# Kernel tuning notes

Measured on AMD Instinct MI355X. Metric: run time of the kernel, lower is better.

The kernel has to match this reference:

```python
import jax, jax.numpy as jnp
import numpy as np
import math

D_MODEL = 512
NUM_HEADS = 8
D_HEAD = D_MODEL // NUM_HEADS
B, S = 8, 1024


def _rel_shift(pos_score):
    # pos_score: [B, H, S, S] -> Transformer-XL relative shift
    b, h, s1, s2 = pos_score.shape
    padded = jnp.concatenate([jnp.zeros((b, h, s1, 1), pos_score.dtype), pos_score], axis=-1)
    padded = padded.reshape(b, h, s2 + 1, s1)
    return padded[:, :, 1:].reshape(b, h, s1, s2)


def setup_inputs() -> dict:
    key = jax.random.key(0)
    ks = jax.random.split(key, 16)
    scale = 1.0 / math.sqrt(D_MODEL)
    inp = {
        'query': jax.random.normal(ks[0], (B, S, D_MODEL), jnp.float32),
        'key': jax.random.normal(ks[1], (B, S, D_MODEL), jnp.float32),
        'value': jax.random.normal(ks[2], (B, S, D_MODEL), jnp.float32),
        'position_emb': jax.random.normal(ks[3], (B, S, D_MODEL), jnp.float32),
        'Wq': jax.random.normal(ks[4], (D_MODEL, D_MODEL), jnp.float32) * scale,
        'bq': jnp.zeros((D_MODEL,), jnp.float32),
        'Wk': jax.random.normal(ks[5], (D_MODEL, D_MODEL), jnp.float32) * scale,
        'bk': jnp.zeros((D_MODEL,), jnp.float32),
        'Wv': jax.random.normal(ks[6], (D_MODEL, D_MODEL), jnp.float32) * scale,
        'bv': jnp.zeros((D_MODEL,), jnp.float32),
        'Wp': jax.random.normal(ks[7], (D_MODEL, D_MODEL), jnp.float32) * scale,
        'u_bias': jax.random.normal(ks[8], (NUM_HEADS, D_HEAD), jnp.float32) * 0.1,
        'v_bias': jax.random.normal(ks[9], (NUM_HEADS, D_HEAD), jnp.float32) * 0.1,
        'Wo': jax.random.normal(ks[10], (D_MODEL, D_MODEL), jnp.float32) * scale,
        'bo': jnp.zeros((D_MODEL,), jnp.float32),
    }
    return inp


def reference(query, key, value, position_emb, Wq, bq, Wk, bk, Wv, bv, Wp, u_bias, v_bias, Wo, bo):
    b, s, _ = query.shape
    q = (query @ Wq + bq).reshape(b, s, NUM_HEADS, D_HEAD)       # [B,S,H,Dh]
    k = (key @ Wk + bk).reshape(b, s, NUM_HEADS, D_HEAD)
    v = (value @ Wv + bv).reshape(b, s, NUM_HEADS, D_HEAD)
    p = (position_emb @ Wp).reshape(b, s, NUM_HEADS, D_HEAD)
    # content score: (q + u) k^T ; pos score: (q + v) p^T with relative shift
    content_score = jnp.einsum('bqhd,bkhd->bhqk', q + u_bias, k)
    pos_score = _rel_shift(jnp.einsum('bqhd,bkhd->bhqk', q + v_bias, p))
    score = (content_score + pos_score) / math.sqrt(D_MODEL)
    atten = jax.nn.softmax(score, axis=-1)                        # dropout off (eval)
    context = jnp.einsum('bhqk,bkhd->bqhd', atten, v).reshape(b, s, D_MODEL)
    return context @ Wo + bo
```

## Files before the change

kernel.cpp:

```cpp
#include <hip/hip_runtime.h>
#include <cstdint>

typedef unsigned short ushort_t;
typedef __attribute__((ext_vector_type(8))) short bf16x8;
typedef __attribute__((ext_vector_type(4))) float f32x4;

#define S_LEN 1024
#define DHEAD 64

__device__ inline ushort_t f2bf(float f) {
    union { float f; uint32_t u; } c; c.f = f;
    uint32_t u = c.u;
    uint32_t r = u + 0x7FFFu + ((u >> 16) & 1u);
    return (ushort_t)(r >> 16);
}
__device__ inline float bf2f(ushort_t h) {
    union { uint32_t u; float f; } c; c.u = ((uint32_t)h) << 16;
    return c.f;
}
__device__ inline bf16x8 load8(const ushort_t* p) {
    union { uint4 u; bf16x8 v; } c;
    c.u = *reinterpret_cast<const uint4*>(p);
    return c.v;
}

__global__ __launch_bounds__(256) void prep_w(
    const float* __restrict__ wq, const float* __restrict__ wk,
    const float* __restrict__ wv, const float* __restrict__ wp,
    const float* __restrict__ wo, ushort_t* __restrict__ ws) {
    __shared__ float tile[64][65];
    int wi = blockIdx.z;
    const float* src = wi == 0 ? wq : wi == 1 ? wk : wi == 2 ? wv : wi == 3 ? wp : wo;
    int cx = blockIdx.x * 64, ry = blockIdx.y * 64;
    int t = threadIdx.x;
    int tr = t >> 4, tc = (t & 15) * 4;
#pragma unroll
    for (int i = 0; i < 4; i++) {
        int r = tr + i * 16;
        float4 f = *reinterpret_cast<const float4*>(src + (size_t)(ry + r) * 512 + cx + tc);
        tile[r][tc] = f.x; tile[r][tc + 1] = f.y; tile[r][tc + 2] = f.z; tile[r][tc + 3] = f.w;
    }
    __syncthreads();
    ushort_t* dst = ws + (size_t)wi * 262144;
#pragma unroll
    for (int i = 0; i < 4; i++) {
        int r = tr + i * 16;
        ushort4 o;
        o.x = f2bf(tile[tc][r]); o.y = f2bf(tile[tc + 1][r]);
        o.z = f2bf(tile[tc + 2][r]); o.w = f2bf(tile[tc + 3][r]);
        *reinterpret_cast<ushort4*>(dst + (size_t)(cx + r) * 512 + ry + tc) = o;
    }
}

__global__ __launch_bounds__(256) void prep_act(
    const float* __restrict__ q, const float* __restrict__ k,
    const float* __restrict__ v, const float* __restrict__ p,
    ushort_t* __restrict__ actb) {
    int t = blockIdx.x * 256 + threadIdx.x;
    int sec = blockIdx.y;
    const float* src = sec == 0 ? q : sec == 1 ? k : sec == 2 ? v : p;
    ushort_t* dst = actb + (size_t)sec * 4194304;
    float4 f = reinterpret_cast<const float4*>(src)[t];
    ushort4 o;
    o.x = f2bf(f.x); o.y = f2bf(f.y); o.z = f2bf(f.z); o.w = f2bf(f.w);
    *reinterpret_cast<ushort4*>(dst + (size_t)t * 4) = o;
}

template<int CVT>
__global__ __launch_bounds__(256) void proj_gemm(
    const float* __restrict__ qa, const float* __restrict__ ka,
    const float* __restrict__ va, const float* __restrict__ pa,
    const ushort_t* __restrict__ actb,
    const ushort_t* __restrict__ wT,
    const float* __restrict__ bq, const float* __restrict__ bk,
    const float* __restrict__ bv,
    const float* __restrict__ ub, const float* __restrict__ vb,
    ushort_t* __restrict__ Qu, ushort_t* __restrict__ Qv,
    ushort_t* __restrict__ Kp, ushort_t* __restrict__ Pp,
    ushort_t* __restrict__ Vt) {
    __shared__ ushort_t smem[2][128][72];
    int z = blockIdx.z;
    const float* Af = z == 0 ? qa : z == 1 ? ka : z == 2 ? pa : va;
    const ushort_t* Ab = actb + (size_t)(z == 0 ? 0 : z == 1 ? 1 : z == 2 ? 3 : 2) * 4194304;
    const ushort_t* Bt = wT + (z == 0 ? 0 : z == 1 ? 262144 : z == 2 ? 786432 : 524288);
    const float* bias = z == 0 ? bq : z == 1 ? bk : z == 3 ? bv : nullptr;

    int tid = threadIdx.x;
    int wid = tid >> 6, lane = tid & 63, quad = lane >> 4, l16 = lane & 15;
    int wr = wid >> 1, wc = wid & 1;
    int row0 = blockIdx.y * 128, col0 = blockIdx.x * 128;

    f32x4 acc[4][4];
#pragma unroll
    for (int i = 0; i < 4; i++)
#pragma unroll
        for (int j = 0; j < 4; j++) acc[i][j] = (f32x4){0.f, 0.f, 0.f, 0.f};

    for (int k0 = 0; k0 < 512; k0 += 64) {
#pragma unroll
        for (int i = 0; i < 4; i++) {
            int cid = tid + i * 256;
            int r = cid >> 3, c8 = cid & 7;
            if (CVT) {
                const float* ap = Af + (size_t)(row0 + r) * 512 + k0 + c8 * 8;
                float4 f0 = *reinterpret_cast<const float4*>(ap);
                float4 f1 = *reinterpret_cast<const float4*>(ap + 4);
                union { ushort_t s[8]; uint4 u; } pk;
                pk.s[0] = f2bf(f0.x); pk.s[1] = f2bf(f0.y); pk.s[2] = f2bf(f0.z); pk.s[3] = f2bf(f0.w);
                pk.s[4] = f2bf(f1.x); pk.s[5] = f2bf(f1.y); pk.s[6] = f2bf(f1.z); pk.s[7] = f2bf(f1.w);
                *reinterpret_cast<uint4*>(&smem[0][r][c8 * 8]) = pk.u;
            } else {
                *reinterpret_cast<uint4*>(&smem[0][r][c8 * 8]) =
                    *reinterpret_cast<const uint4*>(Ab + (size_t)(row0 + r) * 512 + k0 + c8 * 8);
            }
            *reinterpret_cast<uint4*>(&smem[1][r][c8 * 8]) =
                *reinterpret_cast<const uint4*>(Bt + (size_t)(col0 + r) * 512 + k0 + c8 * 8);
        }
        __syncthreads();
#pragma unroll
        for (int kc = 0; kc < 2; kc++) {
            bf16x8 af[4], bg[4];
#pragma unroll
            for (int m = 0; m < 4; m++)
                af[m] = load8(&smem[0][wr * 64 + m * 16 + l16][kc * 32 + quad * 8]);
#pragma unroll
            for (int n = 0; n < 4; n++)
                bg[n] = load8(&smem[1][wc * 64 + n * 16 + l16][kc * 32 + quad * 8]);
#pragma unroll
            for (int m = 0; m < 4; m++)
#pragma unroll
                for (int n = 0; n < 4; n++)
                    acc[m][n] = __builtin_amdgcn_mfma_f32_16x16x32_bf16(af[m], bg[n], acc[m][n], 0, 0, 0);
        }
        __syncthreads();
    }

    if (z == 3) {
        ushort_t (*Ts)[130] = reinterpret_cast<ushort_t(*)[130]>(&smem[0][0][0]);
#pragma unroll
        for (int m = 0; m < 4; m++)
#pragma unroll
            for (int n = 0; n < 4; n++) {
                int dl = wc * 64 + n * 16 + l16;
                float bcol = bv[col0 + dl];
#pragma unroll
                for (int r = 0; r < 4; r++) {
                    int sl = wr * 64 + m * 16 + quad * 4 + r;
                    Ts[dl][sl] = f2bf(acc[m][n][r] + bcol);
                }
            }
        __syncthreads();
        int b_ = row0 >> 10, s0 = row0 & 1023;
#pragma unroll
        for (int p = 0; p < 8; p++) {
            int dl = p * 16 + (tid >> 4);
            int sl = (tid & 15) * 8;
            int col = col0 + dl, h_ = col >> 6, d_ = col & 63;
            ushort_t* dst = Vt + (((size_t)(b_ * 8 + h_)) * 64 + d_) * 1024 + s0 + sl;
            union { uint4 u; ushort_t s[8]; } pk;
#pragma unroll
            for (int e = 0; e < 8; e++) pk.s[e] = Ts[dl][sl + e];
            *reinterpret_cast<uint4*>(dst) = pk.u;
        }
    } else {
#pragma unroll
        for (int m = 0; m < 4; m++)
#pragma unroll
            for (int n = 0; n < 4; n++) {
                int col = col0 + wc * 64 + n * 16 + l16;
                float bcol = bias ? bias[col] : 0.f;
#pragma unroll
                for (int r = 0; r < 4; r++) {
                    int row = row0 + wr * 64 + m * 16 + quad * 4 + r;
                    float val = acc[m][n][r] + bcol;
                    int b_ = row >> 10, s_ = row & 1023, h_ = col >> 6, d_ = col & 63;
                    size_t idx = (((size_t)(b_ * 8 + h_)) * 1024 + s_) * 64 + d_;
                    if (z == 0) {
                        Qu[idx] = f2bf(val + ub[col]);
                        Qv[idx] = f2bf(val + vb[col]);
                    } else {
                        (z == 1 ? Kp : Pp)[idx] = f2bf(val);
                    }
                }
            }
    }
}

__global__ __launch_bounds__(256) void out_gemm(
    const ushort_t* __restrict__ A, const ushort_t* __restrict__ Bt,
    const float* __restrict__ bias, float* __restrict__ outf) {
    __shared__ ushort_t As[128][72];
    __shared__ ushort_t Bs[64][72];
    int tid = threadIdx.x;
    int wid = tid >> 6, lane = tid & 63, quad = lane >> 4, l16 = lane & 15;
    int row0 = blockIdx.y * 128, col0 = blockIdx.x * 64;

    f32x4 acc[2][4];
#pragma unroll
    for (int i = 0; i < 2; i++)
#pragma unroll
        for (int j = 0; j < 4; j++) acc[i][j] = (f32x4){0.f, 0.f, 0.f, 0.f};

    for (int k0 = 0; k0 < 512; k0 += 64) {
#pragma unroll
        for (int i = 0; i < 4; i++) {
            int cid = tid + i * 256;
            int r = cid >> 3, c8 = cid & 7;
            *reinterpret_cast<uint4*>(&As[r][c8 * 8]) =
                *reinterpret_cast<const uint4*>(A + (size_t)(row0 + r) * 512 + k0 + c8 * 8);
        }
#pragma unroll
        for (int i = 0; i < 2; i++) {
            int cid = tid + i * 256;
            int r = cid >> 3, c8 = cid & 7;
            *reinterpret_cast<uint4*>(&Bs[r][c8 * 8]) =
                *reinterpret_cast<const uint4*>(Bt + (size_t)(col0 + r) * 512 + k0 + c8 * 8);
        }
        __syncthreads();
#pragma unroll
        for (int kc = 0; kc < 2; kc++) {
            bf16x8 af[2], bg[4];
#pragma unroll
            for (int m = 0; m < 2; m++)
                af[m] = load8(&As[wid * 32 + m * 16 + l16][kc * 32 + quad * 8]);
#pragma unroll
            for (int n = 0; n < 4; n++)
                bg[n] = load8(&Bs[n * 16 + l16][kc * 32 + quad * 8]);
#pragma unroll
            for (int m = 0; m < 2; m++)
#pragma unroll
                for (int n = 0; n < 4; n++)
                    acc[m][n] = __builtin_amdgcn_mfma_f32_16x16x32_bf16(af[m], bg[n], acc[m][n], 0, 0, 0);
        }
        __syncthreads();
    }
#pragma unroll
    for (int m = 0; m < 2; m++)
#pragma unroll
        for (int n = 0; n < 4; n++) {
            int col = col0 + n * 16 + l16;
#pragma unroll
            for (int r = 0; r < 4; r++) {
                int row = row0 + wid * 32 + m * 16 + quad * 4 + r;
                outf[(size_t)row * 512 + col] = acc[m][n][r] + bias[col];
            }
        }
}

#define POS_EMIT(B0_, B1_, WT_) do {                                          \
    f32x4 acc_ = (f32x4){0.f, 0.f, 0.f, 0.f};                                 \
    acc_ = __builtin_amdgcn_mfma_f32_16x16x32_bf16(av[0], (B0_), acc_, 0, 0, 0); \
    acc_ = __builtin_amdgcn_mfma_f32_16x16x32_bf16(av[1], (B1_), acc_, 0, 0, 0); \
    int kb_ = (WT_) + kbb;                                                    \
    if (kb_ >= kw0 && kb_ + 30 < kw1 && (WT_) + 15 <= collim) {               \
        _Pragma("unroll") for (int r_ = 0; r_ < 4; r_++) {                    \
            int m_ = quad * 4 + r_;                                           \
            sc[mtrow + m_][kb_ + m_ + l16] = f2bf(acc_[r_]);                  \
        }                                                                     \
    } else {                                                                  \
        _Pragma("unroll") for (int r_ = 0; r_ < 4; r_++) {                    \
            int m_ = quad * 4 + r_;                                           \
            int k_ = kb_ + m_ + l16;                                          \
            if (k_ >= kw0 && k_ < kw1 && ((WT_) + l16) <= collim)             \
                sc[mtrow + m_][k_] = f2bf(acc_[r_]);                          \
        }                                                                     \
    }                                                                         \
} while (0)

__device__ __forceinline__ void pos_pass(
    const ushort_t* __restrict__ P_b, ushort_t (*sc)[1032],
    const bf16x8* av, int wlo, int whi, int kbb, int collim, int mtrow,
    int kw0, int kw1, int quad, int l16) {
    if (whi < wlo) return;
    int nw = (whi - wlo) / 16 + 1;
    bf16x8 A0, A1, B0, B1;
    {
        int pr = wlo + l16; if (pr > S_LEN - 1) pr = S_LEN - 1;
        A0 = load8(P_b + (size_t)pr * 64 + quad * 8);
        A1 = load8(P_b + (size_t)pr * 64 + 32 + quad * 8);
    }
    if (nw > 1) {
        int pr = wlo + 16 + l16; if (pr > S_LEN - 1) pr = S_LEN - 1;
        B0 = load8(P_b + (size_t)pr * 64 + quad * 8);
        B1 = load8(P_b + (size_t)pr * 64 + 32 + quad * 8);
    }
    int w = 0;
    for (; w + 1 < nw; w += 2) {
        int wtA = wlo + w * 16;
        POS_EMIT(A0, A1, wtA);
        if (w + 2 < nw) {
            int pr = wtA + 32 + l16; if (pr > S_LEN - 1) pr = S_LEN - 1;
            A0 = load8(P_b + (size_t)pr * 64 + quad * 8);
            A1 = load8(P_b + (size_t)pr * 64 + 32 + quad * 8);
        }
        int wtB = wtA + 16;
        POS_EMIT(B0, B1, wtB);
        if (w + 3 < nw) {
            int pr = wtB + 32 + l16; if (pr > S_LEN - 1) pr = S_LEN - 1;
            B0 = load8(P_b + (size_t)pr * 64 + quad * 8);
            B1 = load8(P_b + (size_t)pr * 64 + 32 + quad * 8);
        }
    }
    if (w < nw) {
        int wt = wlo + w * 16;
        POS_EMIT(A0, A1, wt);
    }
}

__global__ __launch_bounds__(256, 2) void attn_kernel(
    const ushort_t* __restrict__ Qu, const ushort_t* __restrict__ Qv,
    const ushort_t* __restrict__ Kp, const ushort_t* __restrict__ Pp,
    const ushort_t* __restrict__ Vt, ushort_t* __restrict__ ctxb) {
    __shared__ ushort_t sc[32][1032];
    __shared__ float red1[4][32];
    __shared__ float red2[32][8];
    __shared__ float rowinv[32];

    constexpr float SCL = (float)(1.4426950408889634 / 22.627416997969522);

    int i = blockIdx.x;
    int bh = (i & 7) * 8 + (i >> 8);
    int q0 = ((i >> 3) & 31) << 5;

    int tid = threadIdx.x, wid = tid >> 6, lane = tid & 63;
    int quad = lane >> 4, l16 = lane & 15;

    const ushort_t* Qu_b = Qu + (size_t)bh * S_LEN * DHEAD;
    const ushort_t* Qv_b = Qv + (size_t)bh * S_LEN * DHEAD;
    const ushort_t* K_b  = Kp + (size_t)bh * S_LEN * DHEAD;
    const ushort_t* P_b  = Pp + (size_t)bh * S_LEN * DHEAD;
    const ushort_t* V_b  = Vt + (size_t)bh * DHEAD * S_LEN;

    int kw0 = wid << 8, kw1 = kw0 + 256;
    int d0 = wid << 4;

    bf16x8 au0[2], au1[2];
#pragma unroll
    for (int kc = 0; kc < 2; kc++) {
        au0[kc] = load8(Qu_b + (size_t)(q0 + l16) * 64 + kc * 32 + quad * 8);
        au1[kc] = load8(Qu_b + (size_t)(q0 + 16 + l16) * 64 + kc * 32 + quad * 8);
    }

    if (lane < 32) {
        int kz = q0 + lane + 1;
        if (kz >= kw0 && kz < kw1) sc[lane][kz] = 0;
    }

#pragma unroll
    for (int mt = 0; mt < 2; mt++) {
        int q0m = q0 + mt * 16;
        bf16x8 av1[2], av2[2];
#pragma unroll
        for (int kc = 0; kc < 2; kc++) {
            av1[kc] = load8(Qv_b + (size_t)(q0m + l16) * 64 + kc * 32 + quad * 8);
            int r2 = q0m + 1 + l16; if (r2 > S_LEN - 1) r2 = S_LEN - 1;
            av2[kc] = load8(Qv_b + (size_t)r2 * 64 + kc * 32 + quad * 8);
        }
        int wlo = (S_LEN - 16) - q0m + kw0;
        int d1 = kw1 - 1 - q0m; if (d1 > 0) d1 = 0;
        int whi = (S_LEN - 1) + d1;
        pos_pass(P_b, sc, av1, wlo, whi, q0m - (S_LEN - 1), S_LEN - 1,
                 mt * 16, kw0, kw1, quad, l16);
        int wlo2 = kw0 - q0m - 17; if (wlo2 < 0) wlo2 = 0;
        int whi2 = kw1 - 3 - q0m;
        pos_pass(P_b, sc, av2, wlo2, whi2, q0m + 2, 1 << 30,
                 mt * 16, kw0, kw1, quad, l16);
    }

    float pm0[4] = {-1e30f, -1e30f, -1e30f, -1e30f};
    float pm1[4] = {-1e30f, -1e30f, -1e30f, -1e30f};
    const ushort_t* Kw = K_b + (size_t)kw0 * 64;
#pragma unroll
    for (int nt = 0; nt < 16; ++nt) {
        const ushort_t* kp = Kw + (size_t)(nt * 16 + l16) * 64;
        bf16x8 b0 = load8(kp + quad * 8);
        bf16x8 b1 = load8(kp + 32 + quad * 8);
        int kt = kw0 + nt * 16;
        f32x4 a0, a1;
#pragma unroll
        for (int r = 0; r < 4; r++) {
            a0[r] = bf2f(sc[quad * 4 + r][kt + l16]);
            a1[r] = bf2f(sc[16 + quad * 4 + r][kt + l16]);
        }
        a0 = __builtin_amdgcn_mfma_f32_16x16x32_bf16(au0[0], b0, a0, 0, 0, 0);
        a0 = __builtin_amdgcn_mfma_f32_16x16x32_bf16(au0[1], b1, a0, 0, 0, 0);
        a1 = __builtin_amdgcn_mfma_f32_16x16x32_bf16(au1[0], b0, a1, 0, 0, 0);
        a1 = __builtin_amdgcn_mfma_f32_16x16x32_bf16(au1[1], b1, a1, 0, 0, 0);
#pragma unroll
        for (int r = 0; r < 4; r++) {
            sc[quad * 4 + r][kt + l16] = f2bf(a0[r]);
            sc[16 + quad * 4 + r][kt + l16] = f2bf(a1[r]);
            pm0[r] = fmaxf(pm0[r], a0[r]);
            pm1[r] = fmaxf(pm1[r], a1[r]);
        }
    }
#pragma unroll
    for (int off = 1; off < 16; off <<= 1)
#pragma unroll
        for (int r = 0; r < 4; r++) {
            pm0[r] = fmaxf(pm0[r], __shfl_xor(pm0[r], off));
            pm1[r] = fmaxf(pm1[r], __shfl_xor(pm1[r], off));
        }
    if (l16 == 0) {
#pragma unroll
        for (int r = 0; r < 4; r++) {
            red1[wid][quad * 4 + r] = pm0[r];
            red1[wid][16 + quad * 4 + r] = pm1[r];
        }
    }
    __syncthreads();

    int row = tid & 31, cb = tid >> 5;
    float rm = fmaxf(fmaxf(red1[0][row], red1[1][row]), fmaxf(red1[2][row], red1[3][row]));
    float ssum = 0.f;
    ushort_t* sp = &sc[row][cb * 128];
#pragma unroll
    for (int j = 0; j < 16; j++) {
        union { uint4 u; ushort_t s[8]; } in, out;
        in.u = *reinterpret_cast<uint4*>(sp + j * 8);
#pragma unroll
        for (int e = 0; e < 8; e++) {
            float ev = exp2f((bf2f(in.s[e]) - rm) * SCL);
            out.s[e] = f2bf(ev);
            ssum += ev;
        }
        *reinterpret_cast<uint4*>(sp + j * 8) = out.u;
    }
    red2[row][cb] = ssum;
    __syncthreads();
    if (tid < 32) {
        float s = 0.f;
#pragma unroll
        for (int c = 0; c < 8; c++) s += red2[tid][c];
        rowinv[tid] = 1.0f / s;
    }

    const ushort_t* Vw = V_b + (size_t)(d0 + l16) * 1024;
    f32x4 ac0 = (f32x4){0.f, 0.f, 0.f, 0.f};
    f32x4 ac1 = (f32x4){0.f, 0.f, 0.f, 0.f};
#pragma unroll
    for (int kc = 0; kc < 32; ++kc) {
        bf16x8 b = load8(Vw + kc * 32 + quad * 8);
        bf16x8 a0 = load8(&sc[l16][kc * 32 + quad * 8]);
        bf16x8 a1 = load8(&sc[16 + l16][kc * 32 + quad * 8]);
        ac0 = __builtin_amdgcn_mfma_f32_16x16x32_bf16(a0, b, ac0, 0, 0, 0);
        ac1 = __builtin_amdgcn_mfma_f32_16x16x32_bf16(a1, b, ac1, 0, 0, 0);
    }
    __syncthreads();
    int b_ = bh >> 3, h_ = bh & 7;
#pragma unroll
    for (int r = 0; r < 4; r++) {
        int m = quad * 4 + r;
        ctxb[((size_t)b_ * 1024 + (q0 + m)) * 512 + h_ * 64 + d0 + l16] =
            f2bf(ac0[r] * rowinv[m]);
        ctxb[((size_t)b_ * 1024 + (q0 + 16 + m)) * 512 + h_ * 64 + d0 + l16] =
            f2bf(ac1[r] * rowinv[16 + m]);
    }
}

extern "C" void kernel_launch(void* const* d_in, const int* in_sizes, int n_in,
                              void* d_out, int out_size, void* d_ws, size_t ws_size,
                              hipStream_t stream) {
    const float* q  = (const float*)d_in[0];
    const float* k  = (const float*)d_in[1];
    const float* v  = (const float*)d_in[2];
    const float* pe = (const float*)d_in[3];
    const float* Wq = (const float*)d_in[4];
    const float* bq = (const float*)d_in[5];
    const float* Wk = (const float*)d_in[6];
    const float* bk = (const float*)d_in[7];
    const float* Wv = (const float*)d_in[8];
    const float* bv = (const float*)d_in[9];
    const float* Wp = (const float*)d_in[10];
    const float* ub = (const float*)d_in[11];
    const float* vbias = (const float*)d_in[12];
    const float* Wo = (const float*)d_in[13];
    const float* bo = (const float*)d_in[14];
    float* out = (float*)d_out;
    ushort_t* ws = (ushort_t*)d_ws;

    ushort_t* wT  = ws;
    ushort_t* Qu  = ws + 1310720;
    ushort_t* Qv  = Qu + 4194304;
    ushort_t* Kp  = Qv + 4194304;
    ushort_t* Pp  = Kp + 4194304;
    ushort_t* Vt  = Pp + 4194304;
    ushort_t* actb = Vt + 4194304;
    ushort_t* ctx_big = actb;

    const size_t need_big = (size_t)(1310720 + 9 * 4194304) * 2;
    bool big = ws_size >= need_big;

    prep_w<<<dim3(8, 8, 5), 256, 0, stream>>>(Wq, Wk, Wv, Wp, Wo, wT);
    if (big) {
        prep_act<<<dim3(4096, 4), 256, 0, stream>>>(q, k, v, pe, actb);
        proj_gemm<0><<<dim3(4, 64, 4), 256, 0, stream>>>(q, k, v, pe, actb, wT,
            bq, bk, bv, ub, vbias, Qu, Qv, Kp, Pp, Vt);
        attn_kernel<<<2048, 256, 0, stream>>>(Qu, Qv, Kp, Pp, Vt, ctx_big);
        out_gemm<<<dim3(8, 64), 256, 0, stream>>>(ctx_big, wT + 4 * 262144, bo, out);
    } else {
        ushort_t* ctx = actb;
        proj_gemm<1><<<dim3(4, 64, 4), 256, 0, stream>>>(q, k, v, pe, nullptr, wT,
            bq, bk, bv, ub, vbias, Qu, Qv, Kp, Pp, Vt);
        attn_kernel<<<2048, 256, 0, stream>>>(Qu, Qv, Kp, Pp, Vt, ctx);
        out_gemm<<<dim3(8, 64), 256, 0, stream>>>(ctx, wT + 4 * 262144, bo, out);
    }
}
```

Before: 328.1 us.

## Fuse fp32 conversion into projection, async LDS loads in out_gemm, register softmax

Drops the separate activation-conversion kernel and always converts fp32 inputs to bf16 inside the projection GEMM's tile load, removing one launch and a round trip of bf16 activations through memory. The output GEMM now fills shared memory with direct global-to-LDS async loads, which requires unpadded tiles and may add bank conflicts. The attention kernel keeps score tiles in registers, computes exp and row sums there, and writes only the probabilities to shared memory. This avoids a second read-modify-write pass over the score buffer at the cost of higher register pressure.

```diff
diff --git a/kernel.cpp b/kernel.cpp
--- a/kernel.cpp
+++ b/kernel.cpp
@@ -22,6 +22,11 @@
     union { uint4 u; bf16x8 v; } c;
     c.u = *reinterpret_cast<const uint4*>(p);
     return c.v;
+}
+__device__ __forceinline__ void async16(const ushort_t* g, ushort_t* l) {
+    __builtin_amdgcn_global_load_lds(
+        (const __attribute__((address_space(1))) uint32_t*)(const void*)g,
+        (__attribute__((address_space(3))) uint32_t*)(void*)l, 16, 0, 0);
 }
 
 __global__ __launch_bounds__(256) void prep_w(
@@ -52,25 +57,9 @@
     }
 }
 
-__global__ __launch_bounds__(256) void prep_act(
-    const float* __restrict__ q, const float* __restrict__ k,
-    const float* __restrict__ v, const float* __restrict__ p,
-    ushort_t* __restrict__ actb) {
-    int t = blockIdx.x * 256 + threadIdx.x;
-    int sec = blockIdx.y;
-    const float* src = sec == 0 ? q : sec == 1 ? k : sec == 2 ? v : p;
-    ushort_t* dst = actb + (size_t)sec * 4194304;
-    float4 f = reinterpret_cast<const float4*>(src)[t];
-    ushort4 o;
-    o.x = f2bf(f.x); o.y = f2bf(f.y); o.z = f2bf(f.z); o.w = f2bf(f.w);
-    *reinterpret_cast<ushort4*>(dst + (size_t)t * 4) = o;
-}
-
-template<int CVT>
 __global__ __launch_bounds__(256) void proj_gemm(
     const float* __restrict__ qa, const float* __restrict__ ka,
     const float* __restrict__ va, const float* __restrict__ pa,
-    const ushort_t* __restrict__ actb,
     const ushort_t* __restrict__ wT,
     const float* __restrict__ bq, const float* __restrict__ bk,
     const float* __restrict__ bv,
@@ -81,7 +70,6 @@
     __shared__ ushort_t smem[2][128][72];
     int z = blockIdx.z;
     const float* Af = z == 0 ? qa : z == 1 ? ka : z == 2 ? pa : va;
-    const ushort_t* Ab = actb + (size_t)(z == 0 ? 0 : z == 1 ? 1 : z == 2 ? 3 : 2) * 4194304;
     const ushort_t* Bt = wT + (z == 0 ? 0 : z == 1 ? 262144 : z == 2 ? 786432 : 524288);
     const float* bias = z == 0 ? bq : z == 1 ? bk : z == 3 ? bv : nullptr;
 
@@ -101,18 +89,13 @@
         for (int i = 0; i < 4; i++) {
             int cid = tid + i * 256;
             int r = cid >> 3, c8 = cid & 7;
-            if (CVT) {
-                const float* ap = Af + (size_t)(row0 + r) * 512 + k0 + c8 * 8;
-                float4 f0 = *reinterpret_cast<const float4*>(ap);
-                float4 f1 = *reinterpret_cast<const float4*>(ap + 4);
-                union { ushort_t s[8]; uint4 u; } pk;
-                pk.s[0] = f2bf(f0.x); pk.s[1] = f2bf(f0.y); pk.s[2] = f2bf(f0.z); pk.s[3] = f2bf(f0.w);
-                pk.s[4] = f2bf(f1.x); pk.s[5] = f2bf(f1.y); pk.s[6] = f2bf(f1.z); pk.s[7] = f2bf(f1.w);
-                *reinterpret_cast<uint4*>(&smem[0][r][c8 * 8]) = pk.u;
-            } else {
-                *reinterpret_cast<uint4*>(&smem[0][r][c8 * 8]) =
-                    *reinterpret_cast<const uint4*>(Ab + (size_t)(row0 + r) * 512 + k0 + c8 * 8);
-            }
+            const float* ap = Af + (size_t)(row0 + r) * 512 + k0 + c8 * 8;
+            float4 f0 = *reinterpret_cast<const float4*>(ap);
+            float4 f1 = *reinterpret_cast<const float4*>(ap + 4);
+            union { ushort_t s[8]; uint4 u; } pk;
+            pk.s[0] = f2bf(f0.x); pk.s[1] = f2bf(f0.y); pk.s[2] = f2bf(f0.z); pk.s[3] = f2bf(f0.w);
+            pk.s[4] = f2bf(f1.x); pk.s[5] = f2bf(f1.y); pk.s[6] = f2bf(f1.z); pk.s[7] = f2bf(f1.w);
+            *reinterpret_cast<uint4*>(&smem[0][r][c8 * 8]) = pk.u;
             *reinterpret_cast<uint4*>(&smem[1][r][c8 * 8]) =
                 *reinterpret_cast<const uint4*>(Bt + (size_t)(col0 + r) * 512 + k0 + c8 * 8);
         }
@@ -189,8 +172,8 @@
 __global__ __launch_bounds__(256) void out_gemm(
     const ushort_t* __restrict__ A, const ushort_t* __restrict__ Bt,
     const float* __restrict__ bias, float* __restrict__ outf) {
-    __shared__ ushort_t As[128][72];
-    __shared__ ushort_t Bs[64][72];
+    __shared__ ushort_t As[128][64];
+    __shared__ ushort_t Bs[64][64];
     int tid = threadIdx.x;
     int wid = tid >> 6, lane = tid & 63, quad = lane >> 4, l16 = lane & 15;
     int row0 = blockIdx.y * 128, col0 = blockIdx.x * 64;
@@ -203,18 +186,18 @@
 
     for (int k0 = 0; k0 < 512; k0 += 64) {
 #pragma unroll
-        for (int i = 0; i < 4; i++) {
-            int cid = tid + i * 256;
-            int r = cid >> 3, c8 = cid & 7;
-            *reinterpret_cast<uint4*>(&As[r][c8 * 8]) =
-                *reinterpret_cast<const uint4*>(A + (size_t)(row0 + r) * 512 + k0 + c8 * 8);
-        }
-#pragma unroll
-        for (int i = 0; i < 2; i++) {
-            int cid = tid + i * 256;
-            int r = cid >> 3, c8 = cid & 7;
-            *reinterpret_cast<uint4*>(&Bs[r][c8 * 8]) =
-                *reinterpret_cast<const uint4*>(Bt + (size_t)(col0 + r) * 512 + k0 + c8 * 8);
+        for (int j = 0; j < 4; j++) {
+            int idx = j * 64 + lane;
+            int r = 32 * wid + (idx >> 3);
+            int c = (idx & 7) * 8;
+            async16(A + (size_t)(row0 + r) * 512 + k0 + c, &As[32 * wid][0] + j * 512);
+        }
+#pragma unroll
+        for (int j = 0; j < 2; j++) {
+            int idx = j * 64 + lane;
+            int r = 16 * wid + (idx >> 3);
+            int c = (idx & 7) * 8;
+            async16(Bt + (size_t)(col0 + r) * 512 + k0 + c, &Bs[16 * wid][0] + j * 512);
         }
         __syncthreads();
 #pragma unroll
@@ -313,7 +296,7 @@
     const ushort_t* __restrict__ Vt, ushort_t* __restrict__ ctxb) {
     __shared__ ushort_t sc[32][1032];
     __shared__ float red1[4][32];
-    __shared__ float red2[32][8];
+    __shared__ float red2[4][32];
     __shared__ float rowinv[32];
 
     constexpr float SCL = (float)(1.4426950408889634 / 22.627416997969522);
@@ -367,6 +350,7 @@
                  mt * 16, kw0, kw1, quad, l16);
     }
 
+    f32x4 s0[16], s1[16];
     float pm0[4] = {-1e30f, -1e30f, -1e30f, -1e30f};
     float pm1[4] = {-1e30f, -1e30f, -1e30f, -1e30f};
     const ushort_t* Kw = K_b + (size_t)kw0 * 64;
@@ -386,10 +370,10 @@
         a0 = __builtin_amdgcn_mfma_f32_16x16x32_bf16(au0[1], b1, a0, 0, 0, 0);
         a1 = __builtin_amdgcn_mfma_f32_16x16x32_bf16(au1[0], b0, a1, 0, 0, 0);
         a1 = __builtin_amdgcn_mfma_f32_16x16x32_bf16(au1[1], b1, a1, 0, 0, 0);
-#pragma unroll
-        for (int r = 0; r < 4; r++) {
-            sc[quad * 4 + r][kt + l16] = f2bf(a0[r]);
-            sc[16 + quad * 4 + r][kt + l16] = f2bf(a1[r]);
+        s0[nt] = a0;
+        s1[nt] = a1;
+#pragma unroll
+        for (int r = 0; r < 4; r++) {
             pm0[r] = fmaxf(pm0[r], a0[r]);
             pm1[r] = fmaxf(pm1[r], a1[r]);
         }
@@ -410,29 +394,44 @@
     }
     __syncthreads();
 
-    int row = tid & 31, cb = tid >> 5;
-    float rm = fmaxf(fmaxf(red1[0][row], red1[1][row]), fmaxf(red1[2][row], red1[3][row]));
-    float ssum = 0.f;
-    ushort_t* sp = &sc[row][cb * 128];
-#pragma unroll
-    for (int j = 0; j < 16; j++) {
-        union { uint4 u; ushort_t s[8]; } in, out;
-        in.u = *reinterpret_cast<uint4*>(sp + j * 8);
-#pragma unroll
-        for (int e = 0; e < 8; e++) {
-            float ev = exp2f((bf2f(in.s[e]) - rm) * SCL);
-            out.s[e] = f2bf(ev);
-            ssum += ev;
-        }
-        *reinterpret_cast<uint4*>(sp + j * 8) = out.u;
-    }
-    red2[row][cb] = ssum;
+    float rm0[4], rm1[4], sm0[4], sm1[4];
+#pragma unroll
+    for (int r = 0; r < 4; r++) {
+        int m = quad * 4 + r;
+        rm0[r] = fmaxf(fmaxf(red1[0][m], red1[1][m]), fmaxf(red1[2][m], red1[3][m]));
+        rm1[r] = fmaxf(fmaxf(red1[0][16 + m], red1[1][16 + m]),
+                       fmaxf(red1[2][16 + m], red1[3][16 + m]));
+        sm0[r] = 0.f; sm1[r] = 0.f;
+    }
+#pragma unroll
+    for (int nt = 0; nt < 16; ++nt) {
+        int kt = kw0 + nt * 16;
+#pragma unroll
+        for (int r = 0; r < 4; r++) {
+            float e0 = exp2f((s0[nt][r] - rm0[r]) * SCL);
+            float e1 = exp2f((s1[nt][r] - rm1[r]) * SCL);
+            sm0[r] += e0; sm1[r] += e1;
+            sc[quad * 4 + r][kt + l16] = f2bf(e0);
+            sc[16 + quad * 4 + r][kt + l16] = f2bf(e1);
+        }
+    }
+#pragma unroll
+    for (int off = 1; off < 16; off <<= 1)
+#pragma unroll
+        for (int r = 0; r < 4; r++) {
+            sm0[r] += __shfl_xor(sm0[r], off);
+            sm1[r] += __shfl_xor(sm1[r], off);
+        }
+    if (l16 == 0) {
+#pragma unroll
+        for (int r = 0; r < 4; r++) {
+            red2[wid][quad * 4 + r] = sm0[r];
+            red2[wid][16 + quad * 4 + r] = sm1[r];
+        }
+    }
     __syncthreads();
     if (tid < 32) {
-        float s = 0.f;
-#pragma unroll
-        for (int c = 0; c < 8; c++) s += red2[tid][c];
-        rowinv[tid] = 1.0f / s;
+        rowinv[tid] = 1.0f / (red2[0][tid] + red2[1][tid] + red2[2][tid] + red2[3][tid]);
     }
 
     const ushort_t* Vw = V_b + (size_t)(d0 + l16) * 1024;
@@ -485,24 +484,11 @@
     ushort_t* Kp  = Qv + 4194304;
     ushort_t* Pp  = Kp + 4194304;
     ushort_t* Vt  = Pp + 4194304;
-    ushort_t* actb = Vt + 4194304;
-    ushort_t* ctx_big = actb;
-
-    const size_t need_big = (size_t)(1310720 + 9 * 4194304) * 2;
-    bool big = ws_size >= need_big;
+    ushort_t* ctx = Vt + 4194304;
 
     prep_w<<<dim3(8, 8, 5), 256, 0, stream>>>(Wq, Wk, Wv, Wp, Wo, wT);
-    if (big) {
-        prep_act<<<dim3(4096, 4), 256, 0, stream>>>(q, k, v, pe, actb);
-        proj_gemm<0><<<dim3(4, 64, 4), 256, 0, stream>>>(q, k, v, pe, actb, wT,
-            bq, bk, bv, ub, vbias, Qu, Qv, Kp, Pp, Vt);
-        attn_kernel<<<2048, 256, 0, stream>>>(Qu, Qv, Kp, Pp, Vt, ctx_big);
-        out_gemm<<<dim3(8, 64), 256, 0, stream>>>(ctx_big, wT + 4 * 262144, bo, out);
-    } else {
-        ushort_t* ctx = actb;
-        proj_gemm<1><<<dim3(4, 64, 4), 256, 0, stream>>>(q, k, v, pe, nullptr, wT,
-            bq, bk, bv, ub, vbias, Qu, Qv, Kp, Pp, Vt);
-        attn_kernel<<<2048, 256, 0, stream>>>(Qu, Qv, Kp, Pp, Vt, ctx);
-        out_gemm<<<dim3(8, 64), 256, 0, stream>>>(ctx, wT + 4 * 262144, bo, out);
-    }
-}
+    proj_gemm<<<dim3(4, 64, 4), 256, 0, stream>>>(q, k, v, pe, wT,
+        bq, bk, bv, ub, vbias, Qu, Qv, Kp, Pp, Vt);
+    attn_kernel<<<2048, 256, 0, stream>>>(Qu, Qv, Kp, Pp, Vt, ctx);
+    out_gemm<<<dim3(8, 64), 256, 0, stream>>>(ctx, wT + 4 * 262144, bo, out);
+}
```

New measurement: 323.5 us. Within noise of the previous version (-1.4%).
